# Kernel optimization log

Measured on AMD Instinct MI355X. Metric: run time of the kernel, lower is better.

Reference implementation:

```python
import jax, jax.numpy as jnp
import numpy as np

D_MODEL = 1024
NUM_HEADS = 16
HEAD_DIM = D_MODEL // NUM_HEADS


def setup_inputs() -> dict:
    key = jax.random.key(0)
    ks = jax.random.split(key, 11)
    B, S = 2, 2048
    s = 1.0 / np.sqrt(D_MODEL)
    inp = {
        "query": jax.random.normal(ks[0], (B, S, D_MODEL), jnp.float32),
        "key": jax.random.normal(ks[1], (B, S, D_MODEL), jnp.float32),
        "value": jax.random.normal(ks[2], (B, S, D_MODEL), jnp.float32),
        "Wq": jax.random.normal(ks[3], (D_MODEL, D_MODEL), jnp.float32) * s,
        "bq": jnp.zeros((D_MODEL,), jnp.float32),
        "Wk": jax.random.normal(ks[4], (D_MODEL, D_MODEL), jnp.float32) * s,
        "bk": jnp.zeros((D_MODEL,), jnp.float32),
        "Wv": jax.random.normal(ks[5], (D_MODEL, D_MODEL), jnp.float32) * s,
        "bv": jnp.zeros((D_MODEL,), jnp.float32),
        "Wo": jax.random.normal(ks[6], (D_MODEL, D_MODEL), jnp.float32) * s,
        "bo": jnp.zeros((D_MODEL,), jnp.float32),
    }
    return inp


def _split_heads(x):
    B, S, _ = x.shape
    return x.reshape(B, S, NUM_HEADS, HEAD_DIM).transpose(0, 2, 1, 3)  # [B,H,S,d]


def reference(query, key, value, Wq, bq, Wk, bk, Wv, bv, Wo, bo):
    Q = _split_heads(query @ Wq.T + bq)
    K = _split_heads(key @ Wk.T + bk)
    V = _split_heads(value @ Wv.T + bv)
    scale = 1.0 / jnp.sqrt(jnp.asarray(HEAD_DIM, jnp.float32))
    scores = jnp.einsum("bhqd,bhkd->bhqk", Q, K) * scale  # [B,H,S,S]
    weights = jax.nn.softmax(scores, axis=-1)
    attn = jnp.einsum("bhqk,bhkd->bhqd", weights, V)
    B, H, S, d = attn.shape
    attn = attn.transpose(0, 2, 1, 3).reshape(B, S, H * d)
    return attn @ Wo.T + bo
```

## Files before the change

### kernel.cpp

```cpp
#include <hip/hip_runtime.h>
#include <hip/hip_bf16.h>


typedef unsigned short u16;
typedef __attribute__((ext_vector_type(8))) short short8;
typedef __attribute__((ext_vector_type(4))) float floatx4;

__device__ __forceinline__ float bf2f(u16 x) {
  return __uint_as_float(((unsigned)x) << 16);
}
__device__ __forceinline__ u16 f2bf(float f) {
  unsigned x = __float_as_uint(f);
  return (u16)((x + 0x7fffu + ((x >> 16) & 1u)) >> 16);
}
__device__ __forceinline__ ushort2 pk_bf16(float a, float b) {
  __hip_bfloat162 h2 = __float22bfloat162_rn(make_float2(a, b));
  ushort2 u;
  __builtin_memcpy(&u, &h2, 4);
  return u;
}
#if __has_builtin(__builtin_amdgcn_exp2f)
#define EXP2(x) __builtin_amdgcn_exp2f(x)
#else
#define EXP2(x) exp2f(x)
#endif
__device__ __forceinline__ void gll16(const u16* g, u16* lds) {
  __builtin_amdgcn_global_load_lds((const __attribute__((address_space(1))) void*)g,
                                   (__attribute__((address_space(3))) void*)lds,
                                   16, 0, 0);
}
#define DSFENCE() __asm__ volatile("s_waitcnt lgkmcnt(0)" ::: "memory")

__global__ __launch_bounds__(256) void cvt_kernel(
    const float* __restrict__ q, const float* __restrict__ k, const float* __restrict__ v,
    const float* __restrict__ wq, const float* __restrict__ wk,
    const float* __restrict__ wv, const float* __restrict__ wo,
    const float* __restrict__ bq, const float* __restrict__ bk,
    const float* __restrict__ bv, const float* __restrict__ bo,
    u16* __restrict__ ws) {
  const int i4 = (blockIdx.x * 256 + threadIdx.x) * 4;
  const float* src;
  u16* dst;
  int local;
  if (i4 < 4194304)        { src = q;  dst = ws;            local = i4; }
  else if (i4 < 8388608)   { src = k;  dst = ws + 4194304;  local = i4 - 4194304; }
  else if (i4 < 12582912)  { src = v;  dst = ws + 8388608;  local = i4 - 8388608; }
  else if (i4 < 13631488)  { src = wq; dst = ws + 12582912; local = i4 - 12582912; }
  else if (i4 < 14680064)  { src = wk; dst = ws + 13631488; local = i4 - 13631488; }
  else if (i4 < 15728640)  { src = wv; dst = ws + 14680064; local = i4 - 14680064; }
  else if (i4 < 16777216)  { src = wo; dst = ws + 15728640; local = i4 - 15728640; }
  else if (i4 < 16778240)  { src = bq; dst = ws + 16777216; local = i4 - 16777216; }
  else if (i4 < 16779264)  { src = bk; dst = ws + 16779264; local = i4 - 16778240; }
  else if (i4 < 16780288)  { src = bv; dst = ws + 16781312; local = i4 - 16779264; }
  else                     { src = bo; dst = ws + 16783360; local = i4 - 16780288; }
  const float4 f = *(const float4*)(src + local);
  ushort4 o;
  o.x = f2bf(f.x); o.y = f2bf(f.y); o.z = f2bf(f.z); o.w = f2bf(f.w);
  *(ushort4*)(dst + local) = o;
}

__device__ __forceinline__ void gemm_tile(
    const u16* __restrict__ X, const u16* __restrict__ W,
    const u16* __restrict__ bias, u16* __restrict__ out16, float* __restrict__ out32,
    int row0, int col0, int mode, float oscale, u16* As, u16* Bs) {
  const int tid = threadIdx.x;
  const int w = tid >> 6, l = tid & 63;
  const int lan = l & 15, quad = l >> 4;
  const int wm = w & 1, wn = w >> 1;

  floatx4 acc[4][4];
#pragma unroll
  for (int i = 0; i < 4; ++i)
#pragma unroll
    for (int j = 0; j < 4; ++j) acc[i][j] = (floatx4)0.0f;

  const int r0 = tid >> 2, kq0 = tid & 3;
  const int r1 = (tid + 256) >> 2;
  const int woff = w * 512;
  const u16* Xa0 = X + (size_t)(row0 + r0) * 1024 + kq0 * 8;
  const u16* Xa1 = X + (size_t)(row0 + r1) * 1024 + kq0 * 8;
  const u16* Wb0 = W + (size_t)(col0 + r0) * 1024 + kq0 * 8;
  const u16* Wb1 = W + (size_t)(col0 + r1) * 1024 + kq0 * 8;

#define STAGE(buf, kt)                                         \
  do {                                                         \
    gll16(Xa0 + (kt) * 32, As + (buf) * 4096 + woff);          \
    gll16(Xa1 + (kt) * 32, As + (buf) * 4096 + 2048 + woff);   \
    gll16(Wb0 + (kt) * 32, Bs + (buf) * 4096 + woff);          \
    gll16(Wb1 + (kt) * 32, Bs + (buf) * 4096 + 2048 + woff);   \
  } while (0)

  STAGE(0, 0);
  STAGE(1, 1);
  int cur = 0;
  for (int kt = 0; kt < 32; ++kt) {
    if (kt < 30) {
      const int nb = cur == 0 ? 2 : cur - 1;
      STAGE(nb, kt + 2);
      __asm__ volatile("s_waitcnt vmcnt(8)" ::: "memory");
    } else if (kt == 30) {
      __asm__ volatile("s_waitcnt vmcnt(4)" ::: "memory");
    } else {
      __asm__ volatile("s_waitcnt vmcnt(0)" ::: "memory");
    }
    __builtin_amdgcn_s_barrier();

    const u16* Ab = As + cur * 4096;
    const u16* Bb = Bs + cur * 4096;
    short8 af[4], bfr[4];
#pragma unroll
    for (int i = 0; i < 4; ++i)
      af[i] = *(const short8*)(Ab + (wm * 64 + i * 16 + lan) * 32 + quad * 8);
#pragma unroll
    for (int j = 0; j < 4; ++j)
      bfr[j] = *(const short8*)(Bb + (wn * 64 + j * 16 + lan) * 32 + quad * 8);
    __asm__ volatile("s_waitcnt lgkmcnt(0)" ::: "memory");
    __builtin_amdgcn_s_barrier();

#pragma unroll
    for (int i = 0; i < 4; ++i)
#pragma unroll
      for (int j = 0; j < 4; ++j)
        acc[i][j] = __builtin_amdgcn_mfma_f32_16x16x32_bf16(af[i], bfr[j], acc[i][j], 0, 0, 0);
    cur = cur == 2 ? 0 : cur + 1;
  }
#undef STAGE

#pragma unroll
  for (int i = 0; i < 4; ++i) {
    const int mb = row0 + wm * 64 + i * 16 + quad * 4;
#pragma unroll
    for (int j = 0; j < 4; ++j) {
      const int n = col0 + wn * 64 + j * 16 + lan;
      const float bv = bf2f(bias[n]);
      if (mode == 0) {
#pragma unroll
        for (int r = 0; r < 4; ++r)
          out16[(size_t)(mb + r) * 1024 + n] = f2bf((acc[i][j][r] + bv) * oscale);
      } else if (mode == 1) {
        const int b = mb >> 11;
        const int h = n >> 6, dd = n & 63;
        u16* base = out16 + (size_t)((b * 16 + h) * 64 + dd) * 2048;
#pragma unroll
        for (int r = 0; r < 4; ++r) {
          const int s = (mb + r) & 2047;
          const int sp = (s & ~63) | ((s & 15) * 4 + ((s >> 4) & 3));
          base[sp] = f2bf(acc[i][j][r] + bv);
        }
      } else {
#pragma unroll
        for (int r = 0; r < 4; ++r)
          out32[(size_t)(mb + r) * 1024 + n] = acc[i][j][r] + bv;
      }
    }
  }
}

__global__ __launch_bounds__(256) void qkv_kernel(
    const u16* __restrict__ xq, const u16* __restrict__ xk, const u16* __restrict__ xv,
    const u16* __restrict__ Wq, const u16* __restrict__ Wk, const u16* __restrict__ Wv,
    const u16* __restrict__ bq, const u16* __restrict__ bk, const u16* __restrict__ bv,
    u16* __restrict__ Qo, u16* __restrict__ Ko, u16* __restrict__ Vto) {
  __shared__ __align__(16) u16 As[3 * 4096];
  __shared__ __align__(16) u16 Bs[3 * 4096];
  const int bx = blockIdx.x;
  const int tile_m = bx / 24;
  const int rem = bx - tile_m * 24;
  const int which = rem >> 3;
  const int col0 = (rem & 7) * 128;
  const u16* X = which == 0 ? xq : (which == 1 ? xk : xv);
  const u16* W = which == 0 ? Wq : (which == 1 ? Wk : Wv);
  const u16* bias = which == 0 ? bq : (which == 1 ? bk : bv);
  u16* out = which == 0 ? Qo : (which == 1 ? Ko : Vto);
  const float C = 0.125f * 1.4426950408889634f;
  gemm_tile(X, W, bias, out, nullptr, tile_m * 128, col0, which == 2 ? 1 : 0,
            which == 0 ? C : 1.0f, As, Bs);
}

__global__ __launch_bounds__(256) void proj_kernel(
    const u16* __restrict__ X, const u16* __restrict__ W,
    const u16* __restrict__ bias, float* __restrict__ out) {
  __shared__ __align__(16) u16 As[3 * 4096];
  __shared__ __align__(16) u16 Bs[3 * 4096];
  const int bx = blockIdx.x;
  gemm_tile(X, W, bias, nullptr, out, (bx >> 3) * 128, (bx & 7) * 128, 2, 1.0f, As, Bs);
}

#define FIXMAX 16.0f
#define KPAD 72
__global__ __launch_bounds__(256, 2) void attn_kernel(
    const u16* __restrict__ Q, const u16* __restrict__ K,
    const u16* __restrict__ Vt, u16* __restrict__ O) {
  __shared__ __align__(16) u16 Ks[2][64 * KPAD];
  __shared__ __align__(16) u16 Vs[2][64 * KPAD];
  __shared__ __align__(16) u16 Ps[128 * KPAD];
  const int tid = threadIdx.x;
  const int w = tid >> 6, l = tid & 63;
  const int lan = l & 15, quad = l >> 4;
  const int q0 = blockIdx.x * 128;
  const int bh = blockIdx.y;
  const int b = bh >> 4, h = bh & 15;
  const u16* Qg = Q + (size_t)(b * 2048 + q0) * 1024 + h * 64;
  const u16* Kg = K + (size_t)(b * 2048) * 1024 + h * 64;
  const u16* Vg = Vt + (size_t)((b * 16 + h) * 64) * 2048;

  short8 aq[2][2];
#pragma unroll
  for (int mi = 0; mi < 2; ++mi)
#pragma unroll
    for (int kk = 0; kk < 2; ++kk)
      aq[mi][kk] = *(const short8*)(Qg + (size_t)(w * 32 + mi * 16 + lan) * 1024 +
                                    kk * 32 + quad * 8);

  float lrun[2][4];
  floatx4 oacc[2][4];
#pragma unroll
  for (int mi = 0; mi < 2; ++mi) {
#pragma unroll
    for (int r = 0; r < 4; ++r) lrun[mi][r] = 0.f;
#pragma unroll
    for (int nd = 0; nd < 4; ++nd) oacc[mi][nd] = (floatx4)0.0f;
  }

  const int rowA = tid >> 3, colq = (tid & 7) * 8;
  const int rowB = rowA + 32;

  short8 k0 = *(const short8*)(Kg + (size_t)rowA * 1024 + colq);
  short8 k1 = *(const short8*)(Kg + (size_t)rowB * 1024 + colq);
  short8 v0 = *(const short8*)(Vg + (size_t)rowA * 2048 + colq);
  short8 v1 = *(const short8*)(Vg + (size_t)rowB * 2048 + colq);
  *(short8*)(Ks[0] + rowA * KPAD + colq) = k0;
  *(short8*)(Ks[0] + rowB * KPAD + colq) = k1;
  *(short8*)(Vs[0] + rowA * KPAD + colq) = v0;
  *(short8*)(Vs[0] + rowB * KPAD + colq) = v1;
  __syncthreads();

  for (int kt = 0; kt < 32; ++kt) {
    const int cur = kt & 1;
    if (kt < 31) {
      const int kn = kt + 1;
      k0 = *(const short8*)(Kg + (size_t)(kn * 64 + rowA) * 1024 + colq);
      k1 = *(const short8*)(Kg + (size_t)(kn * 64 + rowB) * 1024 + colq);
      v0 = *(const short8*)(Vg + (size_t)rowA * 2048 + kn * 64 + colq);
      v1 = *(const short8*)(Vg + (size_t)rowB * 2048 + kn * 64 + colq);
    }
    const u16* Kc = Ks[cur];
    const u16* Vc = Vs[cur];

    short8 bkf[4][2];
#pragma unroll
    for (int nj = 0; nj < 4; ++nj)
#pragma unroll
      for (int kk = 0; kk < 2; ++kk)
        bkf[nj][kk] = *(const short8*)(Kc + (nj * 16 + lan) * KPAD + kk * 32 + quad * 8);

    floatx4 sacc[2][4];
#pragma unroll
    for (int mi = 0; mi < 2; ++mi)
#pragma unroll
      for (int nj = 0; nj < 4; ++nj) sacc[mi][nj] = (floatx4)(-FIXMAX);
    __builtin_amdgcn_s_setprio(1);
#pragma unroll
    for (int kk = 0; kk < 2; ++kk)
#pragma unroll
      for (int mi = 0; mi < 2; ++mi)
#pragma unroll
        for (int nj = 0; nj < 4; ++nj)
          sacc[mi][nj] =
              __builtin_amdgcn_mfma_f32_16x16x32_bf16(aq[mi][kk], bkf[nj][kk], sacc[mi][nj], 0, 0, 0);
    __builtin_amdgcn_s_setprio(0);

#pragma unroll
    for (int mi = 0; mi < 2; ++mi)
#pragma unroll
      for (int r = 0; r < 4; ++r) {
        const float p0 = EXP2(sacc[mi][0][r]), p1 = EXP2(sacc[mi][1][r]);
        const float p2 = EXP2(sacc[mi][2][r]), p3 = EXP2(sacc[mi][3][r]);
        lrun[mi][r] += (p0 + p1) + (p2 + p3);
        const ushort2 a01 = pk_bf16(p0, p1);
        const ushort2 a23 = pk_bf16(p2, p3);
        ushort4 pp;
        pp.x = a01.x; pp.y = a01.y; pp.z = a23.x; pp.w = a23.y;
        const int qrow = w * 32 + mi * 16 + quad * 4 + r;
        *(ushort4*)(Ps + qrow * KPAD + lan * 4) = pp;
      }

    short8 vb[4][2];
#pragma unroll
    for (int nd = 0; nd < 4; ++nd)
#pragma unroll
      for (int kk = 0; kk < 2; ++kk)
        vb[nd][kk] = *(const short8*)(Vc + (nd * 16 + lan) * KPAD + kk * 32 + quad * 8);
    DSFENCE();

    short8 pa[2][2];
#pragma unroll
    for (int mi = 0; mi < 2; ++mi)
#pragma unroll
      for (int kk = 0; kk < 2; ++kk)
        pa[mi][kk] = *(const short8*)(Ps + (w * 32 + mi * 16 + lan) * KPAD + kk * 32 + quad * 8);
    __builtin_amdgcn_s_setprio(1);
#pragma unroll
    for (int kk = 0; kk < 2; ++kk)
#pragma unroll
      for (int mi = 0; mi < 2; ++mi)
#pragma unroll
        for (int nd = 0; nd < 4; ++nd)
          oacc[mi][nd] =
              __builtin_amdgcn_mfma_f32_16x16x32_bf16(pa[mi][kk], vb[nd][kk], oacc[mi][nd], 0, 0, 0);
    __builtin_amdgcn_s_setprio(0);

    if (kt < 31) {
      u16* Kn = Ks[cur ^ 1];
      u16* Vn = Vs[cur ^ 1];
      *(short8*)(Kn + rowA * KPAD + colq) = k0;
      *(short8*)(Kn + rowB * KPAD + colq) = k1;
      *(short8*)(Vn + rowA * KPAD + colq) = v0;
      *(short8*)(Vn + rowB * KPAD + colq) = v1;
      __syncthreads();
    }
  }

#pragma unroll
  for (int mi = 0; mi < 2; ++mi)
#pragma unroll
    for (int r = 0; r < 4; ++r) {
      float ls = lrun[mi][r];
#pragma unroll
      for (int d = 1; d < 16; d <<= 1) ls += __shfl_xor(ls, d);
      const float inv = 1.0f / ls;
      const int mg = b * 2048 + q0 + w * 32 + mi * 16 + quad * 4 + r;
#pragma unroll
      for (int nd = 0; nd < 4; ++nd) {
        const int col = h * 64 + nd * 16 + lan;
        O[(size_t)mg * 1024 + col] = f2bf(oacc[mi][nd][r] * inv);
      }
    }
}

extern "C" void kernel_launch(void* const* d_in, const int* in_sizes, int n_in,
                              void* d_out, int out_size, void* d_ws, size_t ws_size,
                              hipStream_t stream) {
  const float* query = (const float*)d_in[0];
  const float* key_ = (const float*)d_in[1];
  const float* value = (const float*)d_in[2];
  const float* Wq = (const float*)d_in[3];
  const float* bq = (const float*)d_in[4];
  const float* Wk = (const float*)d_in[5];
  const float* bk = (const float*)d_in[6];
  const float* Wv = (const float*)d_in[7];
  const float* bv = (const float*)d_in[8];
  const float* Wo = (const float*)d_in[9];
  const float* bo = (const float*)d_in[10];
  float* out = (float*)d_out;

  u16* ws = (u16*)d_ws;
  u16* Xq = ws;
  u16* Xk = ws + 4194304;
  u16* Xv = ws + 8388608;
  u16* cWq = ws + 12582912;
  u16* cWk = ws + 13631488;
  u16* cWv = ws + 14680064;
  u16* cWo = ws + 15728640;
  u16* cbq = ws + 16777216;
  u16* cbk = ws + 16779264;
  u16* cbv = ws + 16781312;
  u16* cbo = ws + 16783360;
  u16* Qw = ws + 17301504;
  u16* Kw = ws + 21495808;
  u16* Vtw = ws + 25690112;
  u16* Ow = ws + 29884416;

  cvt_kernel<<<16388, 256, 0, stream>>>(query, key_, value, Wq, Wk, Wv, Wo,
                                        bq, bk, bv, bo, ws);
  qkv_kernel<<<768, 256, 0, stream>>>(Xq, Xk, Xv, cWq, cWk, cWv, cbq, cbk, cbv,
                                      Qw, Kw, Vtw);
  attn_kernel<<<dim3(16, 32), 256, 0, stream>>>(Qw, Kw, Vtw, Ow);
  proj_kernel<<<256, 256, 0, stream>>>(Ow, cWo, cbo, out);
}
```

Before: 238.6 us.

## Keep attention probabilities in registers via transposed MFMA and remap GEMM tile order

The attention kernel swaps the MFMA operand order so S^T and O^T are computed, which leaves the exponentiated probabilities already in B-operand register layout. The P tile therefore no longer round-trips through LDS and the lgkm fence goes away. To match the new k-ordering inside the packed probability fragments, the V-transpose store permutation in the QKV GEMM is changed. The row sums reduce across quads with two shuffles, and the output is written as 4-wide vectors. Separately, the QKV and projection GEMM block indices are remapped so that consecutive blocks spread across column tiles, which is meant to improve L2 locality or distribution across XCDs.

```diff
diff --git a/kernel.cpp b/kernel.cpp
--- a/kernel.cpp
+++ b/kernel.cpp
@@ -29,7 +29,6 @@
                                    (__attribute__((address_space(3))) void*)lds,
                                    16, 0, 0);
 }
-#define DSFENCE() __asm__ volatile("s_waitcnt lgkmcnt(0)" ::: "memory")
 
 __global__ __launch_bounds__(256) void cvt_kernel(
     const float* __restrict__ q, const float* __restrict__ k, const float* __restrict__ v,
@@ -144,7 +143,9 @@
 #pragma unroll
         for (int r = 0; r < 4; ++r) {
           const int s = (mb + r) & 2047;
-          const int sp = (s & ~63) | ((s & 15) * 4 + ((s >> 4) & 3));
+          const int k = s & 63;
+          const int sp = (s & ~63) | (((k >> 4) & 1) << 5) | (((k >> 2) & 3) << 3) |
+                         (((k >> 5) & 1) << 2) | (k & 3);
           base[sp] = f2bf(acc[i][j][r] + bv);
         }
       } else {
@@ -163,7 +164,8 @@
     u16* __restrict__ Qo, u16* __restrict__ Ko, u16* __restrict__ Vto) {
   __shared__ __align__(16) u16 As[3 * 4096];
   __shared__ __align__(16) u16 Bs[3 * 4096];
-  const int bx = blockIdx.x;
+  const int bx0 = blockIdx.x;
+  const int bx = (bx0 & 7) * 96 + (bx0 >> 3);
   const int tile_m = bx / 24;
   const int rem = bx - tile_m * 24;
   const int which = rem >> 3;
@@ -182,7 +184,8 @@
     const u16* __restrict__ bias, float* __restrict__ out) {
   __shared__ __align__(16) u16 As[3 * 4096];
   __shared__ __align__(16) u16 Bs[3 * 4096];
-  const int bx = blockIdx.x;
+  const int bx0 = blockIdx.x;
+  const int bx = (bx0 & 7) * 32 + (bx0 >> 3);
   gemm_tile(X, W, bias, nullptr, out, (bx >> 3) * 128, (bx & 7) * 128, 2, 1.0f, As, Bs);
 }
 
@@ -193,7 +196,6 @@
     const u16* __restrict__ Vt, u16* __restrict__ O) {
   __shared__ __align__(16) u16 Ks[2][64 * KPAD];
   __shared__ __align__(16) u16 Vs[2][64 * KPAD];
-  __shared__ __align__(16) u16 Ps[128 * KPAD];
   const int tid = threadIdx.x;
   const int w = tid >> 6, l = tid & 63;
   const int lan = l & 15, quad = l >> 4;
@@ -204,23 +206,20 @@
   const u16* Kg = K + (size_t)(b * 2048) * 1024 + h * 64;
   const u16* Vg = Vt + (size_t)((b * 16 + h) * 64) * 2048;
 
-  short8 aq[2][2];
+  short8 qf[2][2];
 #pragma unroll
   for (int mi = 0; mi < 2; ++mi)
 #pragma unroll
     for (int kk = 0; kk < 2; ++kk)
-      aq[mi][kk] = *(const short8*)(Qg + (size_t)(w * 32 + mi * 16 + lan) * 1024 +
+      qf[mi][kk] = *(const short8*)(Qg + (size_t)(w * 32 + mi * 16 + lan) * 1024 +
                                     kk * 32 + quad * 8);
 
-  float lrun[2][4];
+  float lrun[2] = {0.f, 0.f};
   floatx4 oacc[2][4];
 #pragma unroll
-  for (int mi = 0; mi < 2; ++mi) {
-#pragma unroll
-    for (int r = 0; r < 4; ++r) lrun[mi][r] = 0.f;
+  for (int mi = 0; mi < 2; ++mi)
 #pragma unroll
     for (int nd = 0; nd < 4; ++nd) oacc[mi][nd] = (floatx4)0.0f;
-  }
 
   const int rowA = tid >> 3, colq = (tid & 7) * 8;
   const int rowB = rowA + 32;
@@ -247,12 +246,12 @@
     const u16* Kc = Ks[cur];
     const u16* Vc = Vs[cur];
 
-    short8 bkf[4][2];
+    short8 kf[4][2];
 #pragma unroll
     for (int nj = 0; nj < 4; ++nj)
 #pragma unroll
       for (int kk = 0; kk < 2; ++kk)
-        bkf[nj][kk] = *(const short8*)(Kc + (nj * 16 + lan) * KPAD + kk * 32 + quad * 8);
+        kf[nj][kk] = *(const short8*)(Kc + (nj * 16 + lan) * KPAD + kk * 32 + quad * 8);
 
     floatx4 sacc[2][4];
 #pragma unroll
@@ -267,38 +266,44 @@
 #pragma unroll
         for (int nj = 0; nj < 4; ++nj)
           sacc[mi][nj] =
-              __builtin_amdgcn_mfma_f32_16x16x32_bf16(aq[mi][kk], bkf[nj][kk], sacc[mi][nj], 0, 0, 0);
+              __builtin_amdgcn_mfma_f32_16x16x32_bf16(kf[nj][kk], qf[mi][kk], sacc[mi][nj], 0, 0, 0);
     __builtin_amdgcn_s_setprio(0);
 
-#pragma unroll
-    for (int mi = 0; mi < 2; ++mi)
+    short8 vf[4][2];
+#pragma unroll
+    for (int nd = 0; nd < 4; ++nd)
+#pragma unroll
+      for (int kk = 0; kk < 2; ++kk)
+        vf[nd][kk] = *(const short8*)(Vc + (nd * 16 + lan) * KPAD + kk * 32 + quad * 8);
+
+    short8 pb[2][2];
+#pragma unroll
+    for (int mi = 0; mi < 2; ++mi) {
+      float p[4][4];
+#pragma unroll
+      for (int nj = 0; nj < 4; ++nj)
+#pragma unroll
+        for (int r = 0; r < 4; ++r) p[nj][r] = EXP2(sacc[mi][nj][r]);
+      float s01 = 0.f, s23 = 0.f;
 #pragma unroll
       for (int r = 0; r < 4; ++r) {
-        const float p0 = EXP2(sacc[mi][0][r]), p1 = EXP2(sacc[mi][1][r]);
-        const float p2 = EXP2(sacc[mi][2][r]), p3 = EXP2(sacc[mi][3][r]);
-        lrun[mi][r] += (p0 + p1) + (p2 + p3);
-        const ushort2 a01 = pk_bf16(p0, p1);
-        const ushort2 a23 = pk_bf16(p2, p3);
-        ushort4 pp;
-        pp.x = a01.x; pp.y = a01.y; pp.z = a23.x; pp.w = a23.y;
-        const int qrow = w * 32 + mi * 16 + quad * 4 + r;
-        *(ushort4*)(Ps + qrow * KPAD + lan * 4) = pp;
+        s01 += p[0][r] + p[1][r];
+        s23 += p[2][r] + p[3][r];
       }
-
-    short8 vb[4][2];
-#pragma unroll
-    for (int nd = 0; nd < 4; ++nd)
-#pragma unroll
-      for (int kk = 0; kk < 2; ++kk)
-        vb[nd][kk] = *(const short8*)(Vc + (nd * 16 + lan) * KPAD + kk * 32 + quad * 8);
-    DSFENCE();
-
-    short8 pa[2][2];
-#pragma unroll
-    for (int mi = 0; mi < 2; ++mi)
-#pragma unroll
-      for (int kk = 0; kk < 2; ++kk)
-        pa[mi][kk] = *(const short8*)(Ps + (w * 32 + mi * 16 + lan) * KPAD + kk * 32 + quad * 8);
+      lrun[mi] += s01 + s23;
+#pragma unroll
+      for (int kk = 0; kk < 2; ++kk) {
+        const ushort2 w0 = pk_bf16(p[kk][0], p[kk][1]);
+        const ushort2 w1 = pk_bf16(p[kk][2], p[kk][3]);
+        const ushort2 w2 = pk_bf16(p[kk + 2][0], p[kk + 2][1]);
+        const ushort2 w3 = pk_bf16(p[kk + 2][2], p[kk + 2][3]);
+        union { short8 s8; ushort us[8]; } u;
+        u.us[0] = w0.x; u.us[1] = w0.y; u.us[2] = w1.x; u.us[3] = w1.y;
+        u.us[4] = w2.x; u.us[5] = w2.y; u.us[6] = w3.x; u.us[7] = w3.y;
+        pb[mi][kk] = u.s8;
+      }
+    }
+
     __builtin_amdgcn_s_setprio(1);
 #pragma unroll
     for (int kk = 0; kk < 2; ++kk)
@@ -307,7 +312,7 @@
 #pragma unroll
         for (int nd = 0; nd < 4; ++nd)
           oacc[mi][nd] =
-              __builtin_amdgcn_mfma_f32_16x16x32_bf16(pa[mi][kk], vb[nd][kk], oacc[mi][nd], 0, 0, 0);
+              __builtin_amdgcn_mfma_f32_16x16x32_bf16(vf[nd][kk], pb[mi][kk], oacc[mi][nd], 0, 0, 0);
     __builtin_amdgcn_s_setprio(0);
 
     if (kt < 31) {
@@ -322,20 +327,22 @@
   }
 
 #pragma unroll
-  for (int mi = 0; mi < 2; ++mi)
-#pragma unroll
-    for (int r = 0; r < 4; ++r) {
-      float ls = lrun[mi][r];
-#pragma unroll
-      for (int d = 1; d < 16; d <<= 1) ls += __shfl_xor(ls, d);
-      const float inv = 1.0f / ls;
-      const int mg = b * 2048 + q0 + w * 32 + mi * 16 + quad * 4 + r;
-#pragma unroll
-      for (int nd = 0; nd < 4; ++nd) {
-        const int col = h * 64 + nd * 16 + lan;
-        O[(size_t)mg * 1024 + col] = f2bf(oacc[mi][nd][r] * inv);
-      }
-    }
+  for (int mi = 0; mi < 2; ++mi) {
+    float ls = lrun[mi];
+    ls += __shfl_xor(ls, 16);
+    ls += __shfl_xor(ls, 32);
+    const float inv = 1.0f / ls;
+    const int qg = b * 2048 + q0 + w * 32 + mi * 16 + lan;
+#pragma unroll
+    for (int nd = 0; nd < 4; ++nd) {
+      ushort4 ov;
+      ov.x = f2bf(oacc[mi][nd][0] * inv);
+      ov.y = f2bf(oacc[mi][nd][1] * inv);
+      ov.z = f2bf(oacc[mi][nd][2] * inv);
+      ov.w = f2bf(oacc[mi][nd][3] * inv);
+      *(ushort4*)(O + (size_t)qg * 1024 + h * 64 + nd * 16 + quad * 4) = ov;
+    }
+  }
 }
 
 extern "C" void kernel_launch(void* const* d_in, const int* in_sizes, int n_in,
```

New measurement: 239.6 us. About the same (+0.4%).
